# Kernel tuning notes

Measured on AMD Instinct MI355X. Metric: run time of the kernel, lower is better.

## Reference

```python
import jax, jax.numpy as jnp
import numpy as np

B, L, S, H, E, D = 2, 2048, 2048, 16, 64, 64


def setup_inputs() -> dict:
    key = jax.random.key(0)
    ks = jax.random.split(key, 6)
    return {
        "q1": jax.random.normal(ks[0], (B, L, H, E), dtype=jnp.float32),
        "k1": jax.random.normal(ks[1], (B, S, H, E), dtype=jnp.float32),
        "v1": jax.random.normal(ks[2], (B, S, H, D), dtype=jnp.float32),
        "q2": jax.random.normal(ks[3], (B, L, H, E), dtype=jnp.float32),
        "k2": jax.random.normal(ks[4], (B, S, H, E), dtype=jnp.float32),
        "v2": jax.random.normal(ks[5], (B, S, H, D), dtype=jnp.float32),
        "attn_mask": 0,  # accepted but unused by the original forward
    }


def reference(q1, k1, v1, q2, k2, v2, attn_mask):
    # scale = 1/sqrt(E) (self.scale is None in init_kwargs)
    scale = 1.0 / jnp.sqrt(jnp.asarray(q1.shape[-1], dtype=q1.dtype))
    # dual QK scores: [B,H,L,S]
    scores1 = jnp.einsum('blhe,bshe->bhls', q1, k1)
    scores2 = jnp.einsum('blhe,bshe->bhls', q2, k2)
    # eval-mode (dropout disabled for deterministic reference)
    A = jnp.tanh(scores1 * scale) * jax.nn.sigmoid(scores2 * scale)
    # weighted V matmul: [B,L,H,D]
    out = jnp.einsum('bhls,bshd->blhd', A, v1)
    return out
```

## Files before the change

kernel.cpp:

```cpp
#include <hip/hip_runtime.h>

constexpr int Bc = 2, Lc = 2048, Sc = 2048, Hc = 16, Ec = 64, Dc = 64;
constexpr int TILES = Sc / 64;
constexpr int NBH   = Bc * Hc;
constexpr size_t TILE_ELEMS = 4096;
constexpr size_t ARR_ELEMS  = (size_t)NBH * TILES * TILE_ELEMS;
constexpr size_t WS_NEED    = ARR_ELEMS * 2 * 3;

typedef float          f32x4  __attribute__((ext_vector_type(4)));
typedef float          f32x16 __attribute__((ext_vector_type(16)));
typedef __bf16         bf16x8 __attribute__((ext_vector_type(8)));
typedef unsigned short u16x8  __attribute__((ext_vector_type(8)));
typedef unsigned short u16x4  __attribute__((ext_vector_type(4)));
typedef unsigned int   u32x4  __attribute__((ext_vector_type(4)));

extern "C" __device__ float __ocml_native_exp2_f32(float);

static __device__ __forceinline__ unsigned cvtpk(float lo, float hi) {
    unsigned r;
    asm("v_cvt_pk_bf16_f32 %0, %1, %2" : "=v"(r) : "v"(lo), "v"(hi));
    return r;
}

static __device__ __forceinline__ float fexp2(float x) {
    return __ocml_native_exp2_f32(x);
}

__global__ __launch_bounds__(256) void prepass_kernel(
    const float* __restrict__ k1, const float* __restrict__ k2,
    const float* __restrict__ v1,
    unsigned short* __restrict__ k1b, unsigned short* __restrict__ k2b,
    unsigned short* __restrict__ vb)
{
    __shared__ unsigned short vt[64 * 80];

    const int blk = blockIdx.x;
    const int st  = blk & 31;
    const int bh  = blk >> 5;
    const int b   = bh >> 4, h = bh & 15;
    const int s0  = st * 64;
    const size_t tileo = (size_t)blk * TILE_ELEMS;

    #pragma unroll
    for (int it = 0; it < 2; ++it) {
        int u  = threadIdx.x + it * 256;
        int s  = u >> 3, e8 = u & 7;
        size_t g = ((size_t)((b * Sc + s0 + s) * Hc + h)) * Ec + e8 * 8;

        float4 x0 = *reinterpret_cast<const float4*>(k1 + g);
        float4 x1 = *reinterpret_cast<const float4*>(k1 + g + 4);
        u32x4 o;
        o[0] = cvtpk(x0.x, x0.y); o[1] = cvtpk(x0.z, x0.w);
        o[2] = cvtpk(x1.x, x1.y); o[3] = cvtpk(x1.z, x1.w);
        *reinterpret_cast<u32x4*>(&k1b[tileo + (size_t)(e8 * 64 + s) * 8]) = o;

        x0 = *reinterpret_cast<const float4*>(k2 + g);
        x1 = *reinterpret_cast<const float4*>(k2 + g + 4);
        o[0] = cvtpk(x0.x, x0.y); o[1] = cvtpk(x0.z, x0.w);
        o[2] = cvtpk(x1.x, x1.y); o[3] = cvtpk(x1.z, x1.w);
        *reinterpret_cast<u32x4*>(&k2b[tileo + (size_t)(e8 * 64 + s) * 8]) = o;

        x0 = *reinterpret_cast<const float4*>(v1 + g);
        x1 = *reinterpret_cast<const float4*>(v1 + g + 4);
        o[0] = cvtpk(x0.x, x0.y); o[1] = cvtpk(x0.z, x0.w);
        o[2] = cvtpk(x1.x, x1.y); o[3] = cvtpk(x1.z, x1.w);
        *reinterpret_cast<u32x4*>(&vt[s * 80 + e8 * 8]) = o;
    }
    __syncthreads();

    #pragma unroll
    for (int it = 0; it < 2; ++it) {
        int u  = threadIdx.x + it * 256;
        int d  = u >> 3, sc8 = u & 7;
        u16x8 o;
        #pragma unroll
        for (int j = 0; j < 8; ++j) o[j] = vt[(sc8 * 8 + j) * 80 + d];
        *reinterpret_cast<u16x8*>(&vb[tileo + (size_t)(sc8 * 64 + d) * 8]) = o;
    }
}

__global__ __launch_bounds__(256, 3) void fused_kernel(
    const float* __restrict__ q1, const float* __restrict__ q2,
    const unsigned short* __restrict__ k1b, const unsigned short* __restrict__ k2b,
    const unsigned short* __restrict__ vb, float* __restrict__ out)
{
    __shared__ float mbuf[4 * 1280];

    const int orig    = blockIdx.x;
    const int logical = (orig & 7) * 128 + (orig >> 3);
    const int lblk = logical & 31;
    const int bh   = logical >> 5;
    const int b    = bh >> 4, h = bh & 15;

    const int tid  = threadIdx.x;
    const int w    = tid >> 6;
    const int lane = tid & 63;
    const int l31  = lane & 31;
    const int hi   = lane >> 5;
    const int qsub = w >> 1;
    const int sh   = w & 1;

    constexpr float C1 = 0.36067376022224085f;
    constexpr float C2 = -0.18033688011112043f;
    const int    qrow  = lblk * 64 + qsub * 32 + l31;
    const size_t qbase = ((size_t)((b * Lc + qrow) * Hc + h)) * Ec;
    u32x4 qa1[4], qa2[4];
    #pragma unroll
    for (int es = 0; es < 4; ++es) {
        const float* p1 = q1 + qbase + es * 16 + hi * 8;
        const float* p2 = q2 + qbase + es * 16 + hi * 8;
        float4 x0 = *reinterpret_cast<const float4*>(p1);
        float4 x1 = *reinterpret_cast<const float4*>(p1 + 4);
        qa1[es] = (u32x4){cvtpk(x0.x * C1, x0.y * C1), cvtpk(x0.z * C1, x0.w * C1),
                          cvtpk(x1.x * C1, x1.y * C1), cvtpk(x1.z * C1, x1.w * C1)};
        x0 = *reinterpret_cast<const float4*>(p2);
        x1 = *reinterpret_cast<const float4*>(p2 + 4);
        qa2[es] = (u32x4){cvtpk(x0.x * C2, x0.y * C2), cvtpk(x0.z * C2, x0.w * C2),
                          cvtpk(x1.x * C2, x1.y * C2), cvtpk(x1.z * C2, x1.w * C2)};
    }

    f32x16 acc0 = {}, acc1 = {};

    const unsigned short* k1g = k1b + (size_t)bh * TILES * TILE_ELEMS;
    const unsigned short* k2g = k2b + (size_t)bh * TILES * TILE_ELEMS;
    const unsigned short* vg  = vb  + (size_t)bh * TILES * TILE_ELEMS;

    const int srow = sh * 32 + l31;
    int koff[4];
    #pragma unroll
    for (int es = 0; es < 4; ++es)
        koff[es] = ((es * 2 + hi) * 64 + srow) * 8;

    int voff[4];
    #pragma unroll
    for (int dt = 0; dt < 2; ++dt)
        #pragma unroll
        for (int ks = 0; ks < 2; ++ks)
            voff[dt * 2 + ks] = ((sh * 4 + ks * 2 + hi) * 64 + dt * 32 + l31) * 8;

    u16x8 kf1[4], kf2[4], vfr[4];
    #pragma unroll
    for (int es = 0; es < 4; ++es) {
        kf1[es] = *reinterpret_cast<const u16x8*>(&k1g[koff[es]]);
        kf2[es] = *reinterpret_cast<const u16x8*>(&k2g[koff[es]]);
    }

    for (int st = 0; st < TILES; ++st) {
        f32x16 s1a = {}, s2a = {};
        __builtin_amdgcn_s_setprio(1);
        #pragma unroll
        for (int es = 0; es < 4; ++es) {
            s1a = __builtin_amdgcn_mfma_f32_32x32x16_bf16(
                __builtin_bit_cast(bf16x8, kf1[es]), __builtin_bit_cast(bf16x8, qa1[es]), s1a, 0, 0, 0);
            s2a = __builtin_amdgcn_mfma_f32_32x32x16_bf16(
                __builtin_bit_cast(bf16x8, kf2[es]), __builtin_bit_cast(bf16x8, qa2[es]), s2a, 0, 0, 0);
        }
        __builtin_amdgcn_s_setprio(0);

        const unsigned short* vt = vg + (size_t)st * TILE_ELEMS;
        #pragma unroll
        for (int i = 0; i < 4; ++i)
            vfr[i] = *reinterpret_cast<const u16x8*>(&vt[voff[i]]);

        if (st + 1 < TILES) {
            const unsigned short* kn1 = k1g + (size_t)(st + 1) * TILE_ELEMS;
            const unsigned short* kn2 = k2g + (size_t)(st + 1) * TILE_ELEMS;
            #pragma unroll
            for (int es = 0; es < 4; ++es) {
                kf1[es] = *reinterpret_cast<const u16x8*>(&kn1[koff[es]]);
                kf2[es] = *reinterpret_cast<const u16x8*>(&kn2[koff[es]]);
            }
        }

        float p[16];
        #pragma unroll
        for (int i = 0; i < 16; ++i) {
            float t  = fexp2(s1a[i]);
            float uu = fexp2(s2a[i]);
            float den = __builtin_fmaf(t, uu, t) + (uu + 1.f);
            p[i] = (t - 1.f) * __builtin_amdgcn_rcpf(den);
        }

        __builtin_amdgcn_s_setprio(1);
        #pragma unroll
        for (int ks = 0; ks < 2; ++ks) {
            unsigned A0 = cvtpk(p[8 * ks + 0], p[8 * ks + 1]);
            unsigned A1 = cvtpk(p[8 * ks + 2], p[8 * ks + 3]);
            unsigned B0 = cvtpk(p[8 * ks + 4], p[8 * ks + 5]);
            unsigned B1 = cvtpk(p[8 * ks + 6], p[8 * ks + 7]);
            asm("v_permlane32_swap_b32 %0, %1" : "+v"(A0), "+v"(B0));
            asm("v_permlane32_swap_b32 %0, %1" : "+v"(A1), "+v"(B1));
            bf16x8 pa = __builtin_bit_cast(bf16x8, (u32x4){A0, A1, B0, B1});
            acc0 = __builtin_amdgcn_mfma_f32_32x32x16_bf16(pa, __builtin_bit_cast(bf16x8, vfr[ks]),     acc0, 0, 0, 0);
            acc1 = __builtin_amdgcn_mfma_f32_32x32x16_bf16(pa, __builtin_bit_cast(bf16x8, vfr[2 + ks]), acc1, 0, 0, 0);
        }
        __builtin_amdgcn_s_setprio(0);
    }

    __syncthreads();
    if (sh == 1) {
        #pragma unroll
        for (int r4 = 0; r4 < 4; ++r4) {
            *reinterpret_cast<f32x4*>(&mbuf[(qsub * 2 + 0) * 1280 + lane * 20 + r4 * 4]) =
                (f32x4){acc0[r4 * 4 + 0], acc0[r4 * 4 + 1], acc0[r4 * 4 + 2], acc0[r4 * 4 + 3]};
            *reinterpret_cast<f32x4*>(&mbuf[(qsub * 2 + 1) * 1280 + lane * 20 + r4 * 4]) =
                (f32x4){acc1[r4 * 4 + 0], acc1[r4 * 4 + 1], acc1[r4 * 4 + 2], acc1[r4 * 4 + 3]};
        }
    }
    __syncthreads();
    if (sh == 0) {
        #pragma unroll
        for (int dt = 0; dt < 2; ++dt) {
            float m[16];
            #pragma unroll
            for (int r4 = 0; r4 < 4; ++r4) {
                f32x4 v = *reinterpret_cast<const f32x4*>(&mbuf[(qsub * 2 + dt) * 1280 + lane * 20 + r4 * 4]);
                m[r4 * 4 + 0] = v[0]; m[r4 * 4 + 1] = v[1]; m[r4 * 4 + 2] = v[2]; m[r4 * 4 + 3] = v[3];
            }
            #pragma unroll
            for (int r = 0; r < 16; ++r) {
                float val = m[r] + (dt == 0 ? acc0[r] : acc1[r]);
                int q = lblk * 64 + qsub * 32 + (r & 3) + 8 * (r >> 2) + 4 * hi;
                out[((size_t)(b * Lc + q) * Hc + h) * Dc + dt * 32 + l31] = val;
            }
        }
    }
}

static __device__ __forceinline__ unsigned short f2bf(float f) {
    unsigned u = __builtin_bit_cast(unsigned, f);
    u += 0x7fffu + ((u >> 16) & 1u);
    return (unsigned short)(u >> 16);
}

__global__ __launch_bounds__(256) void fallback_kernel(
    const float* __restrict__ q1, const float* __restrict__ k1,
    const float* __restrict__ v1, const float* __restrict__ q2,
    const float* __restrict__ k2, float* __restrict__ out)
{
    constexpr int KSTR = 72, VSTR = 88, PSTR = 88;
    __shared__ unsigned short k1t[64 * KSTR];
    __shared__ unsigned short k2t[64 * KSTR];
    __shared__ unsigned short vtt[64 * VSTR];
    __shared__ unsigned short pt [4 * 16 * PSTR];

    const int blk  = blockIdx.x;
    const int lblk = blk & 31;
    const int bh   = blk >> 5;
    const int b    = bh >> 4;
    const int h    = bh & 15;
    const int tid  = threadIdx.x;
    const int w    = tid >> 6;
    const int lane = tid & 63;
    const int lr   = lane & 15;
    const int lg   = lane >> 4;

    const int    qrow  = lblk * 64 + w * 16 + lr;
    const size_t qbase = ((size_t)(b * Lc + qrow) * Hc + h) * Ec;
    bf16x8 a1[2], a2[2];
    for (int es = 0; es < 2; ++es) {
        u16x8 t1, t2;
        for (int j = 0; j < 8; ++j) {
            t1[j] = f2bf(q1[qbase + es * 32 + lg * 8 + j]);
            t2[j] = f2bf(q2[qbase + es * 32 + lg * 8 + j]);
        }
        a1[es] = __builtin_bit_cast(bf16x8, t1);
        a2[es] = __builtin_bit_cast(bf16x8, t2);
    }
    f32x4 acc[4];
    for (int i = 0; i < 4; ++i) acc[i] = (f32x4){0.f, 0.f, 0.f, 0.f};
    constexpr float CT = 0.25f, CS = -0.125f;

    for (int s0 = 0; s0 < Sc; s0 += 64) {
        for (int it = 0; it < 4; ++it) {
            int idx = tid + it * 256;
            int sr  = idx >> 4;
            int c4  = (idx & 15) << 2;
            size_t gk = ((size_t)(b * Sc + s0 + sr) * Hc + h) * Ec + c4;
            float4 x1 = *reinterpret_cast<const float4*>(k1 + gk);
            float4 x2 = *reinterpret_cast<const float4*>(k2 + gk);
            float4 xv = *reinterpret_cast<const float4*>(v1 + gk);
            u16x4 o1, o2;
            o1[0]=f2bf(x1.x); o1[1]=f2bf(x1.y); o1[2]=f2bf(x1.z); o1[3]=f2bf(x1.w);
            o2[0]=f2bf(x2.x); o2[1]=f2bf(x2.y); o2[2]=f2bf(x2.z); o2[3]=f2bf(x2.w);
            *reinterpret_cast<u16x4*>(&k1t[sr * KSTR + c4]) = o1;
            *reinterpret_cast<u16x4*>(&k2t[sr * KSTR + c4]) = o2;
            vtt[(c4 + 0) * VSTR + sr] = f2bf(xv.x);
            vtt[(c4 + 1) * VSTR + sr] = f2bf(xv.y);
            vtt[(c4 + 2) * VSTR + sr] = f2bf(xv.z);
            vtt[(c4 + 3) * VSTR + sr] = f2bf(xv.w);
        }
        __syncthreads();
        for (int ct = 0; ct < 4; ++ct) {
            f32x4 s1 = {0.f,0.f,0.f,0.f}, s2 = {0.f,0.f,0.f,0.f};
            for (int es = 0; es < 2; ++es) {
                bf16x8 b1 = __builtin_bit_cast(bf16x8,
                    *reinterpret_cast<const u16x8*>(&k1t[(ct*16 + lr) * KSTR + es*32 + lg*8]));
                bf16x8 b2 = __builtin_bit_cast(bf16x8,
                    *reinterpret_cast<const u16x8*>(&k2t[(ct*16 + lr) * KSTR + es*32 + lg*8]));
                s1 = __builtin_amdgcn_mfma_f32_16x16x32_bf16(a1[es], b1, s1, 0, 0, 0);
                s2 = __builtin_amdgcn_mfma_f32_16x16x32_bf16(a2[es], b2, s2, 0, 0, 0);
            }
            for (int i = 0; i < 4; ++i) {
                float xa = fminf(fmaxf(s1[i] * CT, -30.f), 30.f);
                float xb = fminf(fmaxf(s2[i] * CS, -30.f), 30.f);
                float t  = __expf(xa);
                float u  = __expf(xb);
                float p  = (t - 1.f) * __builtin_amdgcn_rcpf((t + 1.f) * (1.f + u));
                pt[(w*16 + lg*4 + i) * PSTR + ct*16 + lr] = f2bf(p);
            }
        }
        asm volatile("s_waitcnt lgkmcnt(0)" ::: "memory");
        for (int ks = 0; ks < 2; ++ks) {
            bf16x8 pa = __builtin_bit_cast(bf16x8,
                *reinterpret_cast<const u16x8*>(&pt[(w*16 + lr) * PSTR + ks*32 + lg*8]));
            for (int dt = 0; dt < 4; ++dt) {
                bf16x8 vf = __builtin_bit_cast(bf16x8,
                    *reinterpret_cast<const u16x8*>(&vtt[(dt*16 + lr) * VSTR + ks*32 + lg*8]));
                acc[dt] = __builtin_amdgcn_mfma_f32_16x16x32_bf16(pa, vf, acc[dt], 0, 0, 0);
            }
        }
        __syncthreads();
    }
    const int orow = lblk * 64 + w * 16;
    for (int dt = 0; dt < 4; ++dt)
        for (int i = 0; i < 4; ++i) {
            int l = orow + lg * 4 + i;
            out[((size_t)(b * Lc + l) * Hc + h) * Dc + dt * 16 + lr] = acc[dt][i];
        }
}

extern "C" void kernel_launch(void* const* d_in, const int* in_sizes, int n_in,
                              void* d_out, int out_size, void* d_ws, size_t ws_size,
                              hipStream_t stream) {
    const float* q1 = (const float*)d_in[0];
    const float* k1 = (const float*)d_in[1];
    const float* v1 = (const float*)d_in[2];
    const float* q2 = (const float*)d_in[3];
    const float* k2 = (const float*)d_in[4];
    float* out = (float*)d_out;

    if (ws_size >= WS_NEED) {
        unsigned short* k1b = (unsigned short*)d_ws;
        unsigned short* k2b = k1b + ARR_ELEMS;
        unsigned short* vbp = k2b + ARR_ELEMS;
        prepass_kernel<<<dim3(NBH * TILES), dim3(256), 0, stream>>>(k1, k2, v1, k1b, k2b, vbp);
        fused_kernel<<<dim3(NBH * TILES), dim3(256), 0, stream>>>(q1, q2, k1b, k2b, vbp, out);
    } else {
        fallback_kernel<<<dim3(NBH * TILES), dim3(256), 0, stream>>>(q1, k1, v1, q2, k2, out);
    }
}
```

Baseline: 111.0 us.

## Switch fused kernel to 16x16x32 MFMA with 32-row query blocks

Rewrites the fused attention kernel to use 16x16x32 bf16 MFMA tiles, with each block covering 32 query rows instead of 64. This doubles the grid to 2048 blocks, and the occupancy hint rises to 4 blocks per CU. The epilogue uses smaller per-thread accumulators and a smaller shared reduction buffer. The elementwise gate batches reciprocals, sharing one rcp across four values. The aim is more parallelism and occupancy and less register pressure. In exchange, each block re-reads K and V twice as often per query row and gets less reuse per MFMA.

```diff
diff --git a/kernel.cpp b/kernel.cpp
--- a/kernel.cpp
+++ b/kernel.cpp
@@ -8,7 +8,6 @@
 constexpr size_t WS_NEED    = ARR_ELEMS * 2 * 3;
 
 typedef float          f32x4  __attribute__((ext_vector_type(4)));
-typedef float          f32x16 __attribute__((ext_vector_type(16)));
 typedef __bf16         bf16x8 __attribute__((ext_vector_type(8)));
 typedef unsigned short u16x8  __attribute__((ext_vector_type(8)));
 typedef unsigned short u16x4  __attribute__((ext_vector_type(4)));
@@ -79,149 +78,159 @@
     }
 }
 
-__global__ __launch_bounds__(256, 3) void fused_kernel(
+__global__ __launch_bounds__(256, 4) void fused_kernel(
     const float* __restrict__ q1, const float* __restrict__ q2,
     const unsigned short* __restrict__ k1b, const unsigned short* __restrict__ k2b,
     const unsigned short* __restrict__ vb, float* __restrict__ out)
 {
-    __shared__ float mbuf[4 * 1280];
+    __shared__ float mbuf[2][1092];
 
     const int orig    = blockIdx.x;
-    const int logical = (orig & 7) * 128 + (orig >> 3);
-    const int lblk = logical & 31;
-    const int bh   = logical >> 5;
+    const int logical = (orig & 7) * 256 + (orig >> 3);
+    const int lblk = logical & 63;
+    const int bh   = logical >> 6;
     const int b    = bh >> 4, h = bh & 15;
 
     const int tid  = threadIdx.x;
     const int w    = tid >> 6;
     const int lane = tid & 63;
-    const int l31  = lane & 31;
-    const int hi   = lane >> 5;
+    const int lr   = lane & 15;
+    const int lg   = lane >> 4;
     const int qsub = w >> 1;
     const int sh   = w & 1;
 
     constexpr float C1 = 0.36067376022224085f;
     constexpr float C2 = -0.18033688011112043f;
-    const int    qrow  = lblk * 64 + qsub * 32 + l31;
+    const int    qrow  = lblk * 32 + qsub * 16 + lr;
     const size_t qbase = ((size_t)((b * Lc + qrow) * Hc + h)) * Ec;
-    u32x4 qa1[4], qa2[4];
-    #pragma unroll
-    for (int es = 0; es < 4; ++es) {
-        const float* p1 = q1 + qbase + es * 16 + hi * 8;
-        const float* p2 = q2 + qbase + es * 16 + hi * 8;
+    u32x4 qa1[2], qa2[2];
+    #pragma unroll
+    for (int ec = 0; ec < 2; ++ec) {
+        const float* p1 = q1 + qbase + ec * 32 + lg * 8;
+        const float* p2 = q2 + qbase + ec * 32 + lg * 8;
         float4 x0 = *reinterpret_cast<const float4*>(p1);
         float4 x1 = *reinterpret_cast<const float4*>(p1 + 4);
-        qa1[es] = (u32x4){cvtpk(x0.x * C1, x0.y * C1), cvtpk(x0.z * C1, x0.w * C1),
+        qa1[ec] = (u32x4){cvtpk(x0.x * C1, x0.y * C1), cvtpk(x0.z * C1, x0.w * C1),
                           cvtpk(x1.x * C1, x1.y * C1), cvtpk(x1.z * C1, x1.w * C1)};
         x0 = *reinterpret_cast<const float4*>(p2);
         x1 = *reinterpret_cast<const float4*>(p2 + 4);
-        qa2[es] = (u32x4){cvtpk(x0.x * C2, x0.y * C2), cvtpk(x0.z * C2, x0.w * C2),
+        qa2[ec] = (u32x4){cvtpk(x0.x * C2, x0.y * C2), cvtpk(x0.z * C2, x0.w * C2),
                           cvtpk(x1.x * C2, x1.y * C2), cvtpk(x1.z * C2, x1.w * C2)};
     }
 
-    f32x16 acc0 = {}, acc1 = {};
+    f32x4 acc[4] = {{0.f,0.f,0.f,0.f},{0.f,0.f,0.f,0.f},
+                    {0.f,0.f,0.f,0.f},{0.f,0.f,0.f,0.f}};
 
     const unsigned short* k1g = k1b + (size_t)bh * TILES * TILE_ELEMS;
     const unsigned short* k2g = k2b + (size_t)bh * TILES * TILE_ELEMS;
     const unsigned short* vg  = vb  + (size_t)bh * TILES * TILE_ELEMS;
 
-    const int srow = sh * 32 + l31;
     int koff[4];
     #pragma unroll
-    for (int es = 0; es < 4; ++es)
-        koff[es] = ((es * 2 + hi) * 64 + srow) * 8;
+    for (int st2 = 0; st2 < 2; ++st2)
+        #pragma unroll
+        for (int ec = 0; ec < 2; ++ec)
+            koff[st2 * 2 + ec] = ((ec * 4 + lg) * 64 + sh * 32 + st2 * 16 + lr) * 8;
 
     int voff[4];
     #pragma unroll
-    for (int dt = 0; dt < 2; ++dt)
-        #pragma unroll
-        for (int ks = 0; ks < 2; ++ks)
-            voff[dt * 2 + ks] = ((sh * 4 + ks * 2 + hi) * 64 + dt * 32 + l31) * 8;
+    for (int dt = 0; dt < 4; ++dt)
+        voff[dt] = ((sh * 4 + lg) * 64 + dt * 16 + lr) * 8;
 
     u16x8 kf1[4], kf2[4], vfr[4];
     #pragma unroll
-    for (int es = 0; es < 4; ++es) {
-        kf1[es] = *reinterpret_cast<const u16x8*>(&k1g[koff[es]]);
-        kf2[es] = *reinterpret_cast<const u16x8*>(&k2g[koff[es]]);
+    for (int i = 0; i < 4; ++i) {
+        kf1[i] = *reinterpret_cast<const u16x8*>(&k1g[koff[i]]);
+        kf2[i] = *reinterpret_cast<const u16x8*>(&k2g[koff[i]]);
     }
 
     for (int st = 0; st < TILES; ++st) {
-        f32x16 s1a = {}, s2a = {};
+        f32x4 s1[2] = {{0.f,0.f,0.f,0.f},{0.f,0.f,0.f,0.f}};
+        f32x4 s2[2] = {{0.f,0.f,0.f,0.f},{0.f,0.f,0.f,0.f}};
         __builtin_amdgcn_s_setprio(1);
         #pragma unroll
-        for (int es = 0; es < 4; ++es) {
-            s1a = __builtin_amdgcn_mfma_f32_32x32x16_bf16(
-                __builtin_bit_cast(bf16x8, kf1[es]), __builtin_bit_cast(bf16x8, qa1[es]), s1a, 0, 0, 0);
-            s2a = __builtin_amdgcn_mfma_f32_32x32x16_bf16(
-                __builtin_bit_cast(bf16x8, kf2[es]), __builtin_bit_cast(bf16x8, qa2[es]), s2a, 0, 0, 0);
-        }
+        for (int ec = 0; ec < 2; ++ec)
+            #pragma unroll
+            for (int st2 = 0; st2 < 2; ++st2) {
+                s1[st2] = __builtin_amdgcn_mfma_f32_16x16x32_bf16(
+                    __builtin_bit_cast(bf16x8, kf1[st2 * 2 + ec]),
+                    __builtin_bit_cast(bf16x8, qa1[ec]), s1[st2], 0, 0, 0);
+                s2[st2] = __builtin_amdgcn_mfma_f32_16x16x32_bf16(
+                    __builtin_bit_cast(bf16x8, kf2[st2 * 2 + ec]),
+                    __builtin_bit_cast(bf16x8, qa2[ec]), s2[st2], 0, 0, 0);
+            }
         __builtin_amdgcn_s_setprio(0);
 
         const unsigned short* vt = vg + (size_t)st * TILE_ELEMS;
         #pragma unroll
         for (int i = 0; i < 4; ++i)
             vfr[i] = *reinterpret_cast<const u16x8*>(&vt[voff[i]]);
-
         if (st + 1 < TILES) {
             const unsigned short* kn1 = k1g + (size_t)(st + 1) * TILE_ELEMS;
             const unsigned short* kn2 = k2g + (size_t)(st + 1) * TILE_ELEMS;
             #pragma unroll
-            for (int es = 0; es < 4; ++es) {
-                kf1[es] = *reinterpret_cast<const u16x8*>(&kn1[koff[es]]);
-                kf2[es] = *reinterpret_cast<const u16x8*>(&kn2[koff[es]]);
-            }
-        }
-
-        float p[16];
-        #pragma unroll
-        for (int i = 0; i < 16; ++i) {
-            float t  = fexp2(s1a[i]);
-            float uu = fexp2(s2a[i]);
-            float den = __builtin_fmaf(t, uu, t) + (uu + 1.f);
-            p[i] = (t - 1.f) * __builtin_amdgcn_rcpf(den);
-        }
+            for (int i = 0; i < 4; ++i) {
+                kf1[i] = *reinterpret_cast<const u16x8*>(&kn1[koff[i]]);
+                kf2[i] = *reinterpret_cast<const u16x8*>(&kn2[koff[i]]);
+            }
+        }
+
+        float tt[8], den[8], pv[8];
+        #pragma unroll
+        for (int k = 0; k < 8; ++k) {
+            float a = (k < 4) ? s1[0][k & 3] : s1[1][k & 3];
+            float c = (k < 4) ? s2[0][k & 3] : s2[1][k & 3];
+            float t = fexp2(a);
+            float u = fexp2(c);
+            tt[k]  = t - 1.f;
+            den[k] = __builtin_fmaf(t, u, t) + (u + 1.f);
+        }
+        #pragma unroll
+        for (int g4 = 0; g4 < 8; g4 += 4) {
+            float d01 = den[g4] * den[g4 + 1];
+            float d23 = den[g4 + 2] * den[g4 + 3];
+            float inv = __builtin_amdgcn_rcpf(d01 * d23);
+            float i01 = inv * d23, i23 = inv * d01;
+            pv[g4]     = tt[g4]     * (den[g4 + 1] * i01);
+            pv[g4 + 1] = tt[g4 + 1] * (den[g4]     * i01);
+            pv[g4 + 2] = tt[g4 + 2] * (den[g4 + 3] * i23);
+            pv[g4 + 3] = tt[g4 + 3] * (den[g4 + 2] * i23);
+        }
+
+        unsigned A  = cvtpk(pv[0], pv[1]);
+        unsigned Bw = cvtpk(pv[2], pv[3]);
+        unsigned Cw = cvtpk(pv[4], pv[5]);
+        unsigned Dw = cvtpk(pv[6], pv[7]);
+        asm("v_permlane32_swap_b32 %0, %1" : "+v"(A),  "+v"(Cw));
+        asm("v_permlane32_swap_b32 %0, %1" : "+v"(Bw), "+v"(Dw));
+        asm("v_permlane16_swap_b32 %0, %1" : "+v"(A),  "+v"(Cw));
+        asm("v_permlane16_swap_b32 %0, %1" : "+v"(Bw), "+v"(Dw));
+        bf16x8 pa = __builtin_bit_cast(bf16x8, (u32x4){A, Bw, Cw, Dw});
 
         __builtin_amdgcn_s_setprio(1);
         #pragma unroll
-        for (int ks = 0; ks < 2; ++ks) {
-            unsigned A0 = cvtpk(p[8 * ks + 0], p[8 * ks + 1]);
-            unsigned A1 = cvtpk(p[8 * ks + 2], p[8 * ks + 3]);
-            unsigned B0 = cvtpk(p[8 * ks + 4], p[8 * ks + 5]);
-            unsigned B1 = cvtpk(p[8 * ks + 6], p[8 * ks + 7]);
-            asm("v_permlane32_swap_b32 %0, %1" : "+v"(A0), "+v"(B0));
-            asm("v_permlane32_swap_b32 %0, %1" : "+v"(A1), "+v"(B1));
-            bf16x8 pa = __builtin_bit_cast(bf16x8, (u32x4){A0, A1, B0, B1});
-            acc0 = __builtin_amdgcn_mfma_f32_32x32x16_bf16(pa, __builtin_bit_cast(bf16x8, vfr[ks]),     acc0, 0, 0, 0);
-            acc1 = __builtin_amdgcn_mfma_f32_32x32x16_bf16(pa, __builtin_bit_cast(bf16x8, vfr[2 + ks]), acc1, 0, 0, 0);
-        }
+        for (int dt = 0; dt < 4; ++dt)
+            acc[dt] = __builtin_amdgcn_mfma_f32_16x16x32_bf16(
+                pa, __builtin_bit_cast(bf16x8, vfr[dt]), acc[dt], 0, 0, 0);
         __builtin_amdgcn_s_setprio(0);
     }
 
     __syncthreads();
     if (sh == 1) {
         #pragma unroll
-        for (int r4 = 0; r4 < 4; ++r4) {
-            *reinterpret_cast<f32x4*>(&mbuf[(qsub * 2 + 0) * 1280 + lane * 20 + r4 * 4]) =
-                (f32x4){acc0[r4 * 4 + 0], acc0[r4 * 4 + 1], acc0[r4 * 4 + 2], acc0[r4 * 4 + 3]};
-            *reinterpret_cast<f32x4*>(&mbuf[(qsub * 2 + 1) * 1280 + lane * 20 + r4 * 4]) =
-                (f32x4){acc1[r4 * 4 + 0], acc1[r4 * 4 + 1], acc1[r4 * 4 + 2], acc1[r4 * 4 + 3]};
-        }
+        for (int dt = 0; dt < 4; ++dt)
+            *reinterpret_cast<f32x4*>(&mbuf[qsub][lane * 17 + dt * 4]) = acc[dt];
     }
     __syncthreads();
     if (sh == 0) {
         #pragma unroll
-        for (int dt = 0; dt < 2; ++dt) {
-            float m[16];
+        for (int dt = 0; dt < 4; ++dt) {
+            f32x4 m = *reinterpret_cast<const f32x4*>(&mbuf[qsub][lane * 17 + dt * 4]);
+            m += acc[dt];
             #pragma unroll
-            for (int r4 = 0; r4 < 4; ++r4) {
-                f32x4 v = *reinterpret_cast<const f32x4*>(&mbuf[(qsub * 2 + dt) * 1280 + lane * 20 + r4 * 4]);
-                m[r4 * 4 + 0] = v[0]; m[r4 * 4 + 1] = v[1]; m[r4 * 4 + 2] = v[2]; m[r4 * 4 + 3] = v[3];
-            }
-            #pragma unroll
-            for (int r = 0; r < 16; ++r) {
-                float val = m[r] + (dt == 0 ? acc0[r] : acc1[r]);
-                int q = lblk * 64 + qsub * 32 + (r & 3) + 8 * (r >> 2) + 4 * hi;
-                out[((size_t)(b * Lc + q) * Hc + h) * Dc + dt * 32 + l31] = val;
+            for (int i = 0; i < 4; ++i) {
+                int q = lblk * 32 + qsub * 16 + 4 * lg + i;
+                out[((size_t)(b * Lc + q) * Hc + h) * Dc + dt * 16 + lr] = m[i];
             }
         }
     }
@@ -345,7 +354,7 @@
         unsigned short* k2b = k1b + ARR_ELEMS;
         unsigned short* vbp = k2b + ARR_ELEMS;
         prepass_kernel<<<dim3(NBH * TILES), dim3(256), 0, stream>>>(k1, k2, v1, k1b, k2b, vbp);
-        fused_kernel<<<dim3(NBH * TILES), dim3(256), 0, stream>>>(q1, q2, k1b, k2b, vbp, out);
+        fused_kernel<<<dim3(NBH * 64), dim3(256), 0, stream>>>(q1, q2, k1b, k2b, vbp, out);
     } else {
         fallback_kernel<<<dim3(NBH * TILES), dim3(256), 0, stream>>>(q1, k1, v1, q2, k2, out);
     }
```

Result: slower. 127.6 us (+14.9%).
